# Kernel tuning notes

Measured on AMD Instinct MI355X. Metric: run time of the kernel, lower is better.

The kernel has to match this reference:

```python
import jax, jax.numpy as jnp
import numpy as np

K = 3  # dcn kernel size
PAD = (K - 1) // 2
GRAD_MUL = 0.1


def _deform_conv(x, offsets, weight):
    """DCNv1 (no modulation), stride 1, padding PAD, deformable_groups=1.
    x: [B,C,H,W]; offsets: [B,2*K*K,H,W] with (y,x) pairs per kernel point;
    weight: [O,C,K,K]. Returns [B,O,H,W].
    """
    B, C, H, W = x.shape
    K2 = K * K
    off = offsets.reshape(B, K2, 2, H, W)
    base = jnp.arange(K, dtype=x.dtype) - PAD            # [-1, 0, 1]
    base_y = jnp.repeat(base, K)                          # y repeated
    base_x = jnp.tile(base, K)                            # x tiled
    # sampling coordinates: p0 + pk + offset  -> [B,K2,H,W]
    py = jnp.arange(H, dtype=x.dtype)[None, None, :, None] + base_y[None, :, None, None] + off[:, :, 0]
    px = jnp.arange(W, dtype=x.dtype)[None, None, None, :] + base_x[None, :, None, None] + off[:, :, 1]
    y0 = jnp.floor(py)
    x0 = jnp.floor(px)
    ly = py - y0
    lx = px - x0
    y0i = y0.astype(jnp.int32)
    x0i = x0.astype(jnp.int32)
    x_flat = x.reshape(B, C, H * W)

    def corner(yy, xx, w):
        valid = (yy >= 0) & (yy < H) & (xx >= 0) & (xx < W)
        idx = jnp.clip(yy, 0, H - 1) * W + jnp.clip(xx, 0, W - 1)  # [B,K2,H,W]
        g = jax.vmap(lambda xf, ix: jnp.take(xf, ix.reshape(-1), axis=1))(x_flat, idx)
        g = g.reshape(B, C, K2, H, W)
        return g * (w * valid.astype(x.dtype))[:, None]

    sampled = (corner(y0i, x0i, (1 - ly) * (1 - lx))
               + corner(y0i, x0i + 1, (1 - ly) * lx)
               + corner(y0i + 1, x0i, ly * (1 - lx))
               + corner(y0i + 1, x0i + 1, ly * lx))  # [B,C,K2,H,W]
    w_r = weight.reshape(weight.shape[0], C, K2)
    return jnp.einsum('bckhw,ock->bohw', sampled, w_r)


def setup_inputs() -> dict:
    key = jax.random.key(0)
    k1, k2, k3 = jax.random.split(key, 3)
    B, C, H, W, O = 4, 256, 64, 64, 256
    x = jax.random.normal(k1, (B, C, H, W), dtype=jnp.float32)
    shape_pred = jax.random.normal(k2, (B, 2 * K * K, H, W), dtype=jnp.float32)
    weight = jax.random.normal(k3, (O, C, K, K), dtype=jnp.float32) * 0.01  # normal_init std=0.01
    return {"x": x, "shape_pred": shape_pred, "weight": weight}


def reference(x, shape_pred, weight):
    base = jnp.arange(K, dtype=x.dtype) - PAD
    # dcn_base_offset: (y,x) pairs per kernel point, flattened -> [2*K*K]
    dcn_base = jnp.stack([jnp.repeat(base, K), jnp.tile(base, K)], axis=1).reshape(-1)
    sp = shape_pred * GRAD_MUL + jax.lax.stop_gradient(shape_pred) * (1.0 - GRAD_MUL)
    dcn_offset = sp - dcn_base[None, :, None, None]
    return jax.nn.relu(_deform_conv(x, dcn_offset, weight))
```

## Files before the change

### kernel.cpp

```cpp
#include <hip/hip_runtime.h>
#include <hip/hip_bf16.h>

#define BB 4
#define CC 256
#define HH 64
#define WW 64
#define OO 256
#define NK2 9
#define HWP (HH*WW)
#define KD (NK2*CC)
#define PART_ELEMS (BB*OO*HWP)
#define XT_BYTES   8388608ull
#define WT_BYTES   1179648ull
#define PART_OFF   (XT_BYTES + WT_BYTES)

typedef __bf16 bf16x8 __attribute__((ext_vector_type(8)));
typedef float f32x4 __attribute__((ext_vector_type(4)));
typedef float f32x8 __attribute__((ext_vector_type(8)));
typedef unsigned short u16x8 __attribute__((ext_vector_type(8)));

static __device__ __forceinline__ float bf2f(unsigned short v) {
  return __uint_as_float(((unsigned)v) << 16);
}
static __device__ __forceinline__ unsigned short f2bf(float f) {
  __hip_bfloat16 h = __float2bfloat16(f);
  return __builtin_bit_cast(unsigned short, h);
}

__global__ void k_xpose(const float* __restrict__ x, unsigned short* __restrict__ xt) {
  __shared__ float tile[32][33];
  int b  = blockIdx.z;
  int c0 = blockIdx.y * 32;
  int p0 = blockIdx.x * 32;
  int tx = threadIdx.x & 31;
  int ty = threadIdx.x >> 5;
  const float* src = x + ((size_t)b * CC + c0) * HWP + p0;
#pragma unroll
  for (int i = 0; i < 4; ++i)
    tile[ty + i * 8][tx] = src[(size_t)(ty + i * 8) * HWP + tx];
  __syncthreads();
  unsigned short* dst = xt + ((size_t)b * HWP + p0) * CC + c0;
#pragma unroll
  for (int i = 0; i < 4; ++i) {
    float v = tile[tx][ty + i * 8];
    dst[(size_t)(ty + i * 8) * CC + tx] = f2bf(v);
  }
}

__global__ void k_wt(const float* __restrict__ w, unsigned short* __restrict__ wt) {
  int i = blockIdx.x * 256 + threadIdx.x;
  if (i >= OO * KD) return;
  int kpt = i >> 16;
  int rem = i & 65535;
  int kk = rem >> 13;
  int rem2 = rem & 8191;
  int o = rem2 >> 5;
  int f = rem2 & 31;
  int c = kk * 32 + f;
  wt[i] = f2bf(w[((size_t)o * CC + c) * NK2 + kpt]);
}

template<int KPTN, int NG, int CHN, int BF16OUT>
__launch_bounds__(512)
__global__ void k_dcn(const unsigned short* __restrict__ xt,
                      const unsigned short* __restrict__ wt,
                      const float* __restrict__ sp,
                      void* __restrict__ dstv) {
  constexpr int NKH = 256 / CHN;
  constexpr int RS = CHN * 2;
  constexpr int NCG = CHN / 64;
  constexpr int NKK = CHN / 32;
  __shared__ __align__(16) unsigned short Alds[128 * CHN];

  const int tid = threadIdx.x;
  constexpr int NBLK = NG * NKH * BB * (HH / 2);
  const int hw = blockIdx.x;
  const int swz = (hw & 7) * (NBLK / 8) + (hw >> 3);
  const int gg = swz % (NG * NKH);
  const int gk = gg / NKH;
  const int kh = gg % NKH;
  const int rest = swz / (NG * NKH);
  const int y0 = (rest & 31) * 2;
  const int b = rest >> 5;
  const int kpt0 = gk * KPTN;
  const int cb = kh * CHN;

  const int t8 = tid & 7;
  const int pxb = tid >> 3;

  const int wv = tid >> 6;
  const int lane = tid & 63;
  const int l15 = lane & 15;
  const int lg = lane >> 4;
  const int obase = wv * 32;

  float offY[2][KPTN], offX[2][KPTN];
#pragma unroll
  for (int h = 0; h < 2; ++h)
#pragma unroll
    for (int t = 0; t < KPTN; ++t) {
      offY[h][t] = sp[((size_t)b * 18 + 2 * (kpt0 + t)) * HWP + (y0 + h) * WW + pxb];
      offX[h][t] = sp[((size_t)b * 18 + 2 * (kpt0 + t) + 1) * HWP + (y0 + h) * WW + pxb];
    }

  f32x4 acc[2][8];
#pragma unroll
  for (int i = 0; i < 2; ++i)
#pragma unroll
    for (int j = 0; j < 8; ++j)
      acc[i][j] = (f32x4){0.f, 0.f, 0.f, 0.f};

  const unsigned short* wbase[2];
#pragma unroll
  for (int fm = 0; fm < 2; ++fm)
    wbase[fm] = wt + (size_t)(obase + fm * 16 + l15) * 32 + lg * 8;

  char* Ab = (char*)Alds;
  const unsigned short* xb = xt + (size_t)b * HWP * CC + cb;

#pragma unroll
  for (int t = 0; t < KPTN; ++t) {
    const int kpt = kpt0 + t;
#pragma unroll
    for (int h = 0; h < 2; ++h) {
      const int pm = h * 64 + pxb;
      float py = (float)(y0 + h) + offY[h][t];
      float pxx = (float)pxb + offX[h][t];
      float fy = floorf(py), fx = floorf(pxx);
      float ly = py - fy, lx = pxx - fx;
      int y0i = (int)fy, x0i = (int)fx;
      int y1i = y0i + 1, x1i = x0i + 1;
      bool vy0 = (y0i >= 0) & (y0i < HH);
      bool vy1 = (y1i >= 0) & (y1i < HH);
      bool vx0 = (x0i >= 0) & (x0i < WW);
      bool vx1 = (x1i >= 0) & (x1i < WW);
      float w00 = (1.f - ly) * (1.f - lx);
      float w01 = (1.f - ly) * lx;
      float w10 = ly * (1.f - lx);
      float w11 = ly * lx;
      w00 = (vy0 && vx0) ? w00 : 0.f;
      w01 = (vy0 && vx1) ? w01 : 0.f;
      w10 = (vy1 && vx0) ? w10 : 0.f;
      w11 = (vy1 && vx1) ? w11 : 0.f;
      int yc0 = min(max(y0i, 0), HH - 1), yc1 = min(max(y1i, 0), HH - 1);
      int xc0 = min(max(x0i, 0), WW - 1), xc1 = min(max(x1i, 0), WW - 1);
      const unsigned short* p00 = xb + (yc0 * WW + xc0) * CC + t8 * 8;
      const unsigned short* p01 = xb + (yc0 * WW + xc1) * CC + t8 * 8;
      const unsigned short* p10 = xb + (yc1 * WW + xc0) * CC + t8 * 8;
      const unsigned short* p11 = xb + (yc1 * WW + xc1) * CC + t8 * 8;
#pragma unroll
      for (int cg = 0; cg < NCG; ++cg) {
        u16x8 a00 = *reinterpret_cast<const u16x8*>(p00 + cg * 64);
        u16x8 a01 = *reinterpret_cast<const u16x8*>(p01 + cg * 64);
        u16x8 a10 = *reinterpret_cast<const u16x8*>(p10 + cg * 64);
        u16x8 a11 = *reinterpret_cast<const u16x8*>(p11 + cg * 64);
        u16x8 r;
#pragma unroll
        for (int j = 0; j < 8; ++j) {
          float s = fmaf(w11, bf2f(a11[j]),
                    fmaf(w10, bf2f(a10[j]),
                    fmaf(w01, bf2f(a01[j]), w00 * bf2f(a00[j]))));
          r[j] = f2bf(s);
        }
        unsigned bo = (unsigned)(pm * RS + cg * 128 + t8 * 16) ^ (unsigned)((pm & 7) << 4);
        *reinterpret_cast<u16x8*>(Ab + bo) = r;
      }
    }
    __syncthreads();

#define LOADK(AF, BF, KK)                                                          \
    {                                                                              \
      _Pragma("unroll")                                                            \
      for (int fm = 0; fm < 2; ++fm)                                               \
        AF[fm] = __builtin_bit_cast(bf16x8,                                        \
            *reinterpret_cast<const u16x8*>(wbase[fm] + (size_t)(kpt * 8 + kh * NKK + (KK)) * 8192)); \
      _Pragma("unroll")                                                            \
      for (int fn = 0; fn < 8; ++fn) {                                             \
        int mr = fn * 16 + l15;                                                    \
        unsigned bo = (unsigned)(mr * RS + (KK) * 64 + lg * 16) ^ (unsigned)((mr & 7) << 4); \
        BF[fn] = __builtin_bit_cast(bf16x8, *reinterpret_cast<const u16x8*>(Ab + bo)); \
      }                                                                            \
    }
#define DOMFMA(AF, BF)                                                             \
    {                                                                              \
      _Pragma("unroll")                                                            \
      for (int fm = 0; fm < 2; ++fm)                                               \
        _Pragma("unroll")                                                          \
        for (int fn = 0; fn < 8; ++fn)                                             \
          acc[fm][fn] = __builtin_amdgcn_mfma_f32_16x16x32_bf16(AF[fm], BF[fn], acc[fm][fn], 0, 0, 0); \
    }
    {
      bf16x8 a0[2], a1[2];
      bf16x8 b0[8], b1[8];
      LOADK(a0, b0, 0);
#pragma unroll
      for (int kk = 0; kk < NKK; ++kk) {
        if ((kk & 1) == 0) {
          if (kk < NKK - 1) LOADK(a1, b1, kk + 1);
          DOMFMA(a0, b0);
        } else {
          if (kk < NKK - 1) LOADK(a0, b0, kk + 1);
          DOMFMA(a1, b1);
        }
      }
    }
    __syncthreads();
  }

#pragma unroll
  for (int fm = 0; fm < 2; ++fm) {
#pragma unroll
    for (int fn = 0; fn < 8; ++fn) {
#pragma unroll
      for (int r = 0; r < 4; ++r) {
        int o = obase + fm * 16 + lg * 4 + r;
        int m = fn * 16 + l15;
        int yy = y0 + (m >> 6);
        int xx = m & 63;
        size_t idx = (((size_t)b * OO + o) * HH + yy) * WW + xx;
        float v = acc[fm][fn][r];
        if (BF16OUT) {
          ((unsigned short*)dstv)[(size_t)gg * PART_ELEMS + idx] = f2bf(v);
        } else {
          ((float*)dstv)[idx] = fmaxf(v, 0.0f);
        }
      }
    }
  }
}

template<int NP>
__global__ void k_reduceN(const unsigned short* __restrict__ parts, float* __restrict__ out, int n8) {
  int i = blockIdx.x * 256 + threadIdx.x;
  if (i >= n8) return;
  const u16x8* p = (const u16x8*)parts;
  f32x8 s;
#pragma unroll
  for (int j = 0; j < 8; ++j) s[j] = 0.0f;
#pragma unroll
  for (int q = 0; q < NP; ++q) {
    u16x8 v = p[i + (size_t)q * (PART_ELEMS / 8)];
#pragma unroll
    for (int j = 0; j < 8; ++j) s[j] += bf2f(v[j]);
  }
  f32x8 o;
#pragma unroll
  for (int j = 0; j < 8; ++j) o[j] = fmaxf(s[j], 0.0f);
  *reinterpret_cast<f32x8*>(out + (size_t)i * 8) = o;
}

extern "C" void kernel_launch(void* const* d_in, const int* in_sizes, int n_in,
                              void* d_out, int out_size, void* d_ws, size_t ws_size,
                              hipStream_t stream) {
  const float* x = (const float*)d_in[0];
  const float* sp = (const float*)d_in[1];
  const float* w = (const float*)d_in[2];
  float* out = (float*)d_out;

  unsigned short* xt = (unsigned short*)d_ws;
  unsigned short* wt = (unsigned short*)((char*)d_ws + XT_BYTES);
  unsigned short* parts = (unsigned short*)((char*)d_ws + PART_OFF);

  k_xpose<<<dim3(HWP / 32, CC / 32, BB), 256, 0, stream>>>(x, xt);
  k_wt<<<(OO * KD + 255) / 256, 256, 0, stream>>>(w, wt);

  const size_t need = PART_OFF + 6ull * PART_ELEMS * sizeof(unsigned short);
  if (ws_size >= need) {
    k_dcn<3, 3, 128, 1><<<3 * 2 * BB * (HH / 2), 512, 0, stream>>>(xt, wt, sp, parts);
    k_reduceN<6><<<PART_ELEMS / 8 / 256, 256, 0, stream>>>(parts, out, PART_ELEMS / 8);
  } else {
    k_dcn<9, 1, 256, 0><<<BB * (HH / 2), 512, 0, stream>>>(xt, wt, sp, out);
  }
}
```

Baseline: 63.75 us.

## Add 1024-thread DCN kernel with 4-row tiles and 4-way channel split

Adds a new deformable-conv kernel, launched as 256 blocks of 1024 threads. Each block samples a 4-row by 64-pixel tile over all 9 kernel points for one 64-channel slice, giving a 4-way channel split instead of the earlier 6-way point/channel split. The result is fewer partial-sum buffers for the reduction and larger M tiles for better weight reuse, at the cost of occupancy (one block per CU) and a per-kernel-point sync loop without double buffering. The fallback kernel also drops its precomputed offsets and the register double-buffering of fragments, reading offsets inline.

```diff
diff --git a/kernel.cpp b/kernel.cpp
--- a/kernel.cpp
+++ b/kernel.cpp
@@ -60,6 +60,128 @@
   wt[i] = f2bf(w[((size_t)o * CC + c) * NK2 + kpt]);
 }
 
+__launch_bounds__(1024, 1)
+__global__ void k_dcn2(const unsigned short* __restrict__ xt,
+                       const unsigned short* __restrict__ wt,
+                       const float* __restrict__ sp,
+                       unsigned short* __restrict__ parts) {
+  __shared__ __align__(16) unsigned short Alds[256 * 64];
+
+  const int tid = threadIdx.x;
+  const int bid = blockIdx.x;
+  const int swz = (bid & 7) * 32 + (bid >> 3);
+  const int kh = swz & 3;
+  const int tile = swz >> 2;
+  const int y0 = (tile & 15) * 4;
+  const int b = tile >> 4;
+
+  const int t8 = tid & 7;
+  const int grp = tid >> 3;
+
+  const int wv = tid >> 6;
+  const int wo = wv & 3;
+  const int wm = wv >> 2;
+  const int lane = tid & 63;
+  const int l15 = lane & 15;
+  const int lg = lane >> 4;
+
+  f32x4 acc[4][4];
+#pragma unroll
+  for (int i = 0; i < 4; ++i)
+#pragma unroll
+    for (int j = 0; j < 4; ++j)
+      acc[i][j] = (f32x4){0.f, 0.f, 0.f, 0.f};
+
+  char* Ab = (char*)Alds;
+  const unsigned short* xb = xt + (size_t)b * HWP * CC + kh * 64;
+  const float* spb = sp + (size_t)b * 18 * HWP;
+
+  for (int kpt = 0; kpt < NK2; ++kpt) {
+#pragma unroll
+    for (int pi = 0; pi < 2; ++pi) {
+      const int pp = grp + pi * 128;
+      const int yim = y0 + (pp >> 6);
+      const int xim = pp & 63;
+      float offY = spb[(2 * kpt) * HWP + yim * WW + xim];
+      float offX = spb[(2 * kpt + 1) * HWP + yim * WW + xim];
+      float py = (float)yim + offY;
+      float px = (float)xim + offX;
+      float fy = floorf(py), fx = floorf(px);
+      float ly = py - fy, lx = px - fx;
+      int y0i = (int)fy, x0i = (int)fx;
+      int y1i = y0i + 1, x1i = x0i + 1;
+      bool vy0 = (y0i >= 0) & (y0i < HH);
+      bool vy1 = (y1i >= 0) & (y1i < HH);
+      bool vx0 = (x0i >= 0) & (x0i < WW);
+      bool vx1 = (x1i >= 0) & (x1i < WW);
+      float w00 = (1.f - ly) * (1.f - lx);
+      float w01 = (1.f - ly) * lx;
+      float w10 = ly * (1.f - lx);
+      float w11 = ly * lx;
+      w00 = (vy0 && vx0) ? w00 : 0.f;
+      w01 = (vy0 && vx1) ? w01 : 0.f;
+      w10 = (vy1 && vx0) ? w10 : 0.f;
+      w11 = (vy1 && vx1) ? w11 : 0.f;
+      int yc0 = min(max(y0i, 0), HH - 1), yc1 = min(max(y1i, 0), HH - 1);
+      int xc0 = min(max(x0i, 0), WW - 1), xc1 = min(max(x1i, 0), WW - 1);
+      const unsigned short* q = xb + t8 * 8;
+      u16x8 a00 = *reinterpret_cast<const u16x8*>(q + (yc0 * WW + xc0) * CC);
+      u16x8 a01 = *reinterpret_cast<const u16x8*>(q + (yc0 * WW + xc1) * CC);
+      u16x8 a10 = *reinterpret_cast<const u16x8*>(q + (yc1 * WW + xc0) * CC);
+      u16x8 a11 = *reinterpret_cast<const u16x8*>(q + (yc1 * WW + xc1) * CC);
+      u16x8 r;
+#pragma unroll
+      for (int j = 0; j < 8; ++j) {
+        float s = fmaf(w11, bf2f(a11[j]),
+                  fmaf(w10, bf2f(a10[j]),
+                  fmaf(w01, bf2f(a01[j]), w00 * bf2f(a00[j]))));
+        r[j] = f2bf(s);
+      }
+      unsigned bo = (unsigned)(pp * 128 + t8 * 16) ^ (unsigned)((pp & 7) << 4);
+      *reinterpret_cast<u16x8*>(Ab + bo) = r;
+    }
+    __syncthreads();
+
+#pragma unroll
+    for (int kk = 0; kk < 2; ++kk) {
+      bf16x8 afr[4], bfr[4];
+#pragma unroll
+      for (int fm = 0; fm < 4; ++fm)
+        afr[fm] = __builtin_bit_cast(bf16x8, *reinterpret_cast<const u16x8*>(
+            wt + (size_t)(kpt * 8 + kh * 2 + kk) * 8192
+               + (wo * 64 + fm * 16 + l15) * 32 + lg * 8));
+#pragma unroll
+      for (int fn = 0; fn < 4; ++fn) {
+        int mr = wm * 64 + fn * 16 + l15;
+        unsigned bo = (unsigned)(mr * 128 + kk * 64 + lg * 16) ^ (unsigned)((mr & 7) << 4);
+        bfr[fn] = __builtin_bit_cast(bf16x8, *reinterpret_cast<const u16x8*>(Ab + bo));
+      }
+#pragma unroll
+      for (int fm = 0; fm < 4; ++fm)
+#pragma unroll
+        for (int fn = 0; fn < 4; ++fn)
+          acc[fm][fn] = __builtin_amdgcn_mfma_f32_16x16x32_bf16(afr[fm], bfr[fn], acc[fm][fn], 0, 0, 0);
+    }
+    __syncthreads();
+  }
+
+  unsigned short* dp = parts + (size_t)kh * PART_ELEMS;
+#pragma unroll
+  for (int fm = 0; fm < 4; ++fm) {
+#pragma unroll
+    for (int fn = 0; fn < 4; ++fn) {
+#pragma unroll
+      for (int r = 0; r < 4; ++r) {
+        int o = wo * 64 + fm * 16 + lg * 4 + r;
+        int m = wm * 64 + fn * 16 + l15;
+        int yy = y0 + (m >> 6);
+        int xx = m & 63;
+        dp[(((size_t)b * OO + o) * HH + yy) * WW + xx] = f2bf(acc[fm][fn][r]);
+      }
+    }
+  }
+}
+
 template<int KPTN, int NG, int CHN, int BF16OUT>
 __launch_bounds__(512)
 __global__ void k_dcn(const unsigned short* __restrict__ xt,
@@ -94,15 +216,6 @@
   const int lg = lane >> 4;
   const int obase = wv * 32;
 
-  float offY[2][KPTN], offX[2][KPTN];
-#pragma unroll
-  for (int h = 0; h < 2; ++h)
-#pragma unroll
-    for (int t = 0; t < KPTN; ++t) {
-      offY[h][t] = sp[((size_t)b * 18 + 2 * (kpt0 + t)) * HWP + (y0 + h) * WW + pxb];
-      offX[h][t] = sp[((size_t)b * 18 + 2 * (kpt0 + t) + 1) * HWP + (y0 + h) * WW + pxb];
-    }
-
   f32x4 acc[2][8];
 #pragma unroll
   for (int i = 0; i < 2; ++i)
@@ -118,14 +231,15 @@
   char* Ab = (char*)Alds;
   const unsigned short* xb = xt + (size_t)b * HWP * CC + cb;
 
-#pragma unroll
   for (int t = 0; t < KPTN; ++t) {
     const int kpt = kpt0 + t;
 #pragma unroll
     for (int h = 0; h < 2; ++h) {
       const int pm = h * 64 + pxb;
-      float py = (float)(y0 + h) + offY[h][t];
-      float pxx = (float)pxb + offX[h][t];
+      float offY = sp[((size_t)b * 18 + 2 * kpt) * HWP + (y0 + h) * WW + pxb];
+      float offX = sp[((size_t)b * 18 + 2 * kpt + 1) * HWP + (y0 + h) * WW + pxb];
+      float py = (float)(y0 + h) + offY;
+      float pxx = (float)pxb + offX;
       float fy = floorf(py), fx = floorf(pxx);
       float ly = py - fy, lx = pxx - fx;
       int y0i = (int)fy, x0i = (int)fx;
@@ -168,41 +282,24 @@
     }
     __syncthreads();
 
-#define LOADK(AF, BF, KK)                                                          \
-    {                                                                              \
-      _Pragma("unroll")                                                            \
-      for (int fm = 0; fm < 2; ++fm)                                               \
-        AF[fm] = __builtin_bit_cast(bf16x8,                                        \
-            *reinterpret_cast<const u16x8*>(wbase[fm] + (size_t)(kpt * 8 + kh * NKK + (KK)) * 8192)); \
-      _Pragma("unroll")                                                            \
-      for (int fn = 0; fn < 8; ++fn) {                                             \
-        int mr = fn * 16 + l15;                                                    \
-        unsigned bo = (unsigned)(mr * RS + (KK) * 64 + lg * 16) ^ (unsigned)((mr & 7) << 4); \
-        BF[fn] = __builtin_bit_cast(bf16x8, *reinterpret_cast<const u16x8*>(Ab + bo)); \
-      }                                                                            \
-    }
-#define DOMFMA(AF, BF)                                                             \
-    {                                                                              \
-      _Pragma("unroll")                                                            \
-      for (int fm = 0; fm < 2; ++fm)                                               \
-        _Pragma("unroll")                                                          \
-        for (int fn = 0; fn < 8; ++fn)                                             \
-          acc[fm][fn] = __builtin_amdgcn_mfma_f32_16x16x32_bf16(AF[fm], BF[fn], acc[fm][fn], 0, 0, 0); \
-    }
-    {
-      bf16x8 a0[2], a1[2];
-      bf16x8 b0[8], b1[8];
-      LOADK(a0, b0, 0);
-#pragma unroll
-      for (int kk = 0; kk < NKK; ++kk) {
-        if ((kk & 1) == 0) {
-          if (kk < NKK - 1) LOADK(a1, b1, kk + 1);
-          DOMFMA(a0, b0);
-        } else {
-          if (kk < NKK - 1) LOADK(a0, b0, kk + 1);
-          DOMFMA(a1, b1);
-        }
-      }
+#pragma unroll
+    for (int kk = 0; kk < NKK; ++kk) {
+      bf16x8 afr[2], bfr[8];
+#pragma unroll
+      for (int fm = 0; fm < 2; ++fm)
+        afr[fm] = __builtin_bit_cast(bf16x8,
+            *reinterpret_cast<const u16x8*>(wbase[fm] + (size_t)(kpt * 8 + kh * NKK + kk) * 8192));
+#pragma unroll
+      for (int fn = 0; fn < 8; ++fn) {
+        int mr = fn * 16 + l15;
+        unsigned bo = (unsigned)(mr * RS + kk * 64 + lg * 16) ^ (unsigned)((mr & 7) << 4);
+        bfr[fn] = __builtin_bit_cast(bf16x8, *reinterpret_cast<const u16x8*>(Ab + bo));
+      }
+#pragma unroll
+      for (int fm = 0; fm < 2; ++fm)
+#pragma unroll
+        for (int fn = 0; fn < 8; ++fn)
+          acc[fm][fn] = __builtin_amdgcn_mfma_f32_16x16x32_bf16(afr[fm], bfr[fn], acc[fm][fn], 0, 0, 0);
     }
     __syncthreads();
   }
@@ -264,10 +361,10 @@
   k_xpose<<<dim3(HWP / 32, CC / 32, BB), 256, 0, stream>>>(x, xt);
   k_wt<<<(OO * KD + 255) / 256, 256, 0, stream>>>(w, wt);
 
-  const size_t need = PART_OFF + 6ull * PART_ELEMS * sizeof(unsigned short);
+  const size_t need = PART_OFF + 4ull * PART_ELEMS * sizeof(unsigned short);
   if (ws_size >= need) {
-    k_dcn<3, 3, 128, 1><<<3 * 2 * BB * (HH / 2), 512, 0, stream>>>(xt, wt, sp, parts);
-    k_reduceN<6><<<PART_ELEMS / 8 / 256, 256, 0, stream>>>(parts, out, PART_ELEMS / 8);
+    k_dcn2<<<256, 1024, 0, stream>>>(xt, wt, sp, parts);
+    k_reduceN<4><<<PART_ELEMS / 8 / 256, 256, 0, stream>>>(parts, out, PART_ELEMS / 8);
   } else {
     k_dcn<9, 1, 256, 0><<<BB * (HH / 2), 512, 0, stream>>>(xt, wt, sp, out);
   }
```

Measured after the change: 78.96 us. 1.24x slower.
